# Optimization experiments

Hardware: AMD Instinct MI355X
Metric: run time of the kernel (lower is better)

Reference implementation:

```python
import jax, jax.numpy as jnp
import numpy as np

RES = 96
CENTER = RES // 2
EPS = 1e-5


def setup_inputs() -> dict:
    key = jax.random.key(0)
    boundary_2d = jax.random.normal(key, (RES, RES), dtype=jnp.float32)
    return {"boundary_2d": boundary_2d}


def reference(boundary_2d):
    res, center, eps = RES, CENTER, EPS
    idx = jnp.arange(res, dtype=boundary_2d.dtype)
    ii, jj = jnp.meshgrid(idx, idx, indexing="ij")            # [res,res]

    # radius from grid center for every target pixel
    r = jnp.sqrt((ii - center) ** 2 + (jj - center) ** 2)      # [res,res]
    z = center - r + eps                                       # depth into the bulk

    # sources: only strictly-positive boundary values contribute
    w = jnp.where(boundary_2d > 0.0, boundary_2d, 0.0)         # [res,res]

    # all-pairs squared planar distance between targets (i,j) and sources (bi,bj)
    d2 = ((ii[:, :, None, None] - ii[None, None, :, :]) ** 2
          + (jj[:, :, None, None] - jj[None, None, :, :]) ** 2)  # [res,res,res,res]

    # original adds eps to the distance BEFORE squaring: (sqrt(d2)+eps)^2 + z^2
    denom = (jnp.sqrt(d2) + eps) ** 2 + (z ** 2)[:, :, None, None]
    potential = jnp.sum(w[None, None, :, :] / denom, axis=(2, 3))  # [res,res]

    # rim (r >= center-1) passes boundary value through; interior gets the potential
    return jnp.where(r >= center - 1, boundary_2d, potential)
```

## Files before the change

### kernel.cpp

```cpp
#include <hip/hip_runtime.h>

#define RES 96
#define CENTER 48
#define NPIX (RES * RES)
#define EPSF 1e-5f

__global__ __launch_bounds__(256) void topos_kernel(const float* __restrict__ src,
                                                    float* __restrict__ out) {
    const int lane = threadIdx.x & 63;
    const int grp = blockIdx.x * 4 + (threadIdx.x >> 6);
    const int pix0 = grp * 4;
    const int i = pix0 / RES;
    const int j0 = pix0 - i * RES;

    bool rim[4];
    float z2[4];
    bool allrim = true;
    #pragma unroll
    for (int p = 0; p < 4; ++p) {
        const int dj = j0 + p - CENTER;
        const int r2 = (i - CENTER) * (i - CENTER) + dj * dj;
        rim[p] = r2 >= (CENTER - 1) * (CENTER - 1);
        allrim &= rim[p];
        const float z = (float)CENTER - sqrtf((float)r2) + EPSF;
        z2[p] = z * z;
    }

    if (allrim) {
        if (lane == 0) {
            #pragma unroll
            for (int p = 0; p < 4; ++p) out[pix0 + p] = src[pix0 + p];
        }
        return;
    }

    const int s0 = lane * 4;
    const int biq0 = s0 / RES;
    const int bjq0 = s0 - biq0 * RES;
    float fdi = (float)(i - biq0);
    float y = (float)(j0 - bjq0);
    const float wraplim = (float)(j0 - 95);
    const float* ptr = src + s0;

    float acc0 = 0.f, acc1 = 0.f, acc2 = 0.f, acc3 = 0.f;

    #pragma unroll 4
    for (int it = 0; it < NPIX / 256; ++it) {
        const float4 b4 = *(const float4*)ptr;
        ptr += 256;
        const float w0 = fmaxf(b4.x, 0.f);
        const float w1 = fmaxf(b4.y, 0.f);
        const float w2 = fmaxf(b4.z, 0.f);
        const float w3 = fmaxf(b4.w, 0.f);

        const float s2 = fdi * fdi;
        const float vm3 = y - 3.f, vm2 = y - 2.f, vm1 = y - 1.f;
        const float vp1 = y + 1.f, vp2 = y + 2.f, vp3 = y + 3.f;

        {
            const float t = s2 + z2[0];
            const float d0 = fmaf(y, y, t),     d1 = fmaf(vm1, vm1, t);
            const float d2 = fmaf(vm2, vm2, t), d3 = fmaf(vm3, vm3, t);
            const float d01 = d0 * d1, d23 = d2 * d3;
            const float n01 = fmaf(w0, d1, w1 * d0);
            const float n23 = fmaf(w2, d3, w3 * d2);
            acc0 = fmaf(fmaf(n01, d23, n23 * d01),
                        __builtin_amdgcn_rcpf(d01 * d23), acc0);
        }
        {
            const float t = s2 + z2[1];
            const float d0 = fmaf(vp1, vp1, t), d1 = fmaf(y, y, t);
            const float d2 = fmaf(vm1, vm1, t), d3 = fmaf(vm2, vm2, t);
            const float d01 = d0 * d1, d23 = d2 * d3;
            const float n01 = fmaf(w0, d1, w1 * d0);
            const float n23 = fmaf(w2, d3, w3 * d2);
            acc1 = fmaf(fmaf(n01, d23, n23 * d01),
                        __builtin_amdgcn_rcpf(d01 * d23), acc1);
        }
        {
            const float t = s2 + z2[2];
            const float d0 = fmaf(vp2, vp2, t), d1 = fmaf(vp1, vp1, t);
            const float d2 = fmaf(y, y, t),     d3 = fmaf(vm1, vm1, t);
            const float d01 = d0 * d1, d23 = d2 * d3;
            const float n01 = fmaf(w0, d1, w1 * d0);
            const float n23 = fmaf(w2, d3, w3 * d2);
            acc2 = fmaf(fmaf(n01, d23, n23 * d01),
                        __builtin_amdgcn_rcpf(d01 * d23), acc2);
        }
        {
            const float t = s2 + z2[3];
            const float d0 = fmaf(vp3, vp3, t), d1 = fmaf(vp2, vp2, t);
            const float d2 = fmaf(vp1, vp1, t), d3 = fmaf(y, y, t);
            const float d01 = d0 * d1, d23 = d2 * d3;
            const float n01 = fmaf(w0, d1, w1 * d0);
            const float n23 = fmaf(w2, d3, w3 * d2);
            acc3 = fmaf(fmaf(n01, d23, n23 * d01),
                        __builtin_amdgcn_rcpf(d01 * d23), acc3);
        }

        y -= 64.f;
        const bool wr = y < wraplim;
        y = wr ? y + 96.f : y;
        fdi -= wr ? 3.f : 2.f;
    }

    #pragma unroll
    for (int off = 32; off > 0; off >>= 1) {
        acc0 += __shfl_down(acc0, off, 64);
        acc1 += __shfl_down(acc1, off, 64);
        acc2 += __shfl_down(acc2, off, 64);
        acc3 += __shfl_down(acc3, off, 64);
    }

    if (lane == 0) {
        out[pix0 + 0] = rim[0] ? src[pix0 + 0] : acc0;
        out[pix0 + 1] = rim[1] ? src[pix0 + 1] : acc1;
        out[pix0 + 2] = rim[2] ? src[pix0 + 2] : acc2;
        out[pix0 + 3] = rim[3] ? src[pix0 + 3] : acc3;
    }
}

extern "C" void kernel_launch(void* const* d_in, const int* in_sizes, int n_in,
                              void* d_out, int out_size, void* d_ws, size_t ws_size,
                              hipStream_t stream) {
    const float* src = (const float*)d_in[0];
    float* out = (float*)d_out;
    topos_kernel<<<NPIX / 16, 256, 0, stream>>>(src, out);
}
```

Baseline: 65.81 us.

## Split each pixel group's source sum across four waves with LDS reduction

Each block now handles one 4-pixel group, and its four waves each sweep a quarter of the source grid (9 iterations instead of 36). Partial sums are combined through shared memory after a block barrier. This cuts the serial loop length per wave and launches four times as many blocks, which should improve latency hiding and load balance. The cost is extra LDS traffic, a __syncthreads, and four times more blocks to launch and schedule.

```diff
diff --git a/kernel.cpp b/kernel.cpp
--- a/kernel.cpp
+++ b/kernel.cpp
@@ -7,34 +7,32 @@
 
 __global__ __launch_bounds__(256) void topos_kernel(const float* __restrict__ src,
                                                     float* __restrict__ out) {
-    const int lane = threadIdx.x & 63;
-    const int grp = blockIdx.x * 4 + (threadIdx.x >> 6);
-    const int pix0 = grp * 4;
+    const int tid = threadIdx.x;
+    const int wave = tid >> 6;
+    const int lane = tid & 63;
+    const int pix0 = blockIdx.x * 4;
     const int i = pix0 / RES;
     const int j0 = pix0 - i * RES;
 
-    bool rim[4];
+    __shared__ float partial[16];
+
     float z2[4];
     bool allrim = true;
     #pragma unroll
     for (int p = 0; p < 4; ++p) {
         const int dj = j0 + p - CENTER;
         const int r2 = (i - CENTER) * (i - CENTER) + dj * dj;
-        rim[p] = r2 >= (CENTER - 1) * (CENTER - 1);
-        allrim &= rim[p];
+        allrim &= (r2 >= (CENTER - 1) * (CENTER - 1));
         const float z = (float)CENTER - sqrtf((float)r2) + EPSF;
         z2[p] = z * z;
     }
 
     if (allrim) {
-        if (lane == 0) {
-            #pragma unroll
-            for (int p = 0; p < 4; ++p) out[pix0 + p] = src[pix0 + p];
-        }
+        if (tid < 4) out[pix0 + tid] = src[pix0 + tid];
         return;
     }
 
-    const int s0 = lane * 4;
+    const int s0 = wave * 256 + lane * 4;
     const int biq0 = s0 / RES;
     const int bjq0 = s0 - biq0 * RES;
     float fdi = (float)(i - biq0);
@@ -44,10 +42,9 @@
 
     float acc0 = 0.f, acc1 = 0.f, acc2 = 0.f, acc3 = 0.f;
 
-    #pragma unroll 4
-    for (int it = 0; it < NPIX / 256; ++it) {
+    #pragma unroll 3
+    for (int it = 0; it < 9; ++it, ptr += 1024) {
         const float4 b4 = *(const float4*)ptr;
-        ptr += 256;
         const float w0 = fmaxf(b4.x, 0.f);
         const float w1 = fmaxf(b4.y, 0.f);
         const float w2 = fmaxf(b4.z, 0.f);
@@ -101,7 +98,7 @@
         y -= 64.f;
         const bool wr = y < wraplim;
         y = wr ? y + 96.f : y;
-        fdi -= wr ? 3.f : 2.f;
+        fdi -= wr ? 11.f : 10.f;
     }
 
     #pragma unroll
@@ -113,10 +110,20 @@
     }
 
     if (lane == 0) {
-        out[pix0 + 0] = rim[0] ? src[pix0 + 0] : acc0;
-        out[pix0 + 1] = rim[1] ? src[pix0 + 1] : acc1;
-        out[pix0 + 2] = rim[2] ? src[pix0 + 2] : acc2;
-        out[pix0 + 3] = rim[3] ? src[pix0 + 3] : acc3;
+        partial[wave * 4 + 0] = acc0;
+        partial[wave * 4 + 1] = acc1;
+        partial[wave * 4 + 2] = acc2;
+        partial[wave * 4 + 3] = acc3;
+    }
+    __syncthreads();
+
+    if (tid < 4) {
+        const float sum = (partial[tid] + partial[4 + tid])
+                        + (partial[8 + tid] + partial[12 + tid]);
+        const int dj = j0 + tid - CENTER;
+        const int r2 = (i - CENTER) * (i - CENTER) + dj * dj;
+        const bool rim = r2 >= (CENTER - 1) * (CENTER - 1);
+        out[pix0 + tid] = rim ? src[pix0 + tid] : sum;
     }
 }
 
@@ -125,5 +132,5 @@
                               hipStream_t stream) {
     const float* src = (const float*)d_in[0];
     float* out = (float*)d_out;
-    topos_kernel<<<NPIX / 16, 256, 0, stream>>>(src, out);
+    topos_kernel<<<NPIX / 4, 256, 0, stream>>>(src, out);
 }
```

After: 61.53 us. -6.5%, faster.
